# Performance work log

Measured on AMD Instinct MI355X. Metric: run time of the kernel, lower is better.

## Reference

```python
import jax, jax.numpy as jnp
import numpy as np

N_USERS = 100000
N_ITEMS = 50000
N_LAYERS = 3
LATENT_DIM = 64
N_INTERACTIONS = 600000
BATCH = 4096
N_TOTAL = N_USERS + N_ITEMS


def setup_inputs() -> dict:
    key = jax.random.key(0)
    k_e, k_u, k_p, k_n = jax.random.split(key, 4)

    # --- build bipartite interaction graph (numpy, host-side like scipy in the original) ---
    rng = np.random.default_rng(0)
    u = rng.integers(0, N_USERS, size=N_INTERACTIONS)
    i = rng.integers(0, N_ITEMS, size=N_INTERACTIONS) + N_USERS
    # symmetrize: A[u, i] = 1 and A[i, u] = 1
    row = np.concatenate([u, i]).astype(np.int32)
    col = np.concatenate([i, u]).astype(np.int32)
    # symmetric degree normalization: D^{-1/2} A D^{-1/2}
    deg = np.bincount(row, minlength=N_TOTAL).astype(np.float32)
    d_inv = np.power(deg + 1e-9, -0.5)
    d_inv[np.isinf(d_inv)] = 0.0
    vals = (d_inv[row] * d_inv[col]).astype(np.float32)

    # Xavier-uniform init for E0 (fan_in = fan_out = dims of the weight matrix)
    limit = float(np.sqrt(6.0 / (N_TOTAL + LATENT_DIM)))
    E0 = jax.random.uniform(k_e, (N_TOTAL, LATENT_DIM), jnp.float32, -limit, limit)

    return {
        "users": jax.random.randint(k_u, (BATCH,), 0, N_USERS),
        "pos_items": jax.random.randint(k_p, (BATCH,), 0, N_ITEMS),
        "neg_items": jax.random.randint(k_n, (BATCH,), 0, N_ITEMS),
        "E0": E0,
        "adj_row": jnp.asarray(row),
        "adj_col": jnp.asarray(col),
        "adj_vals": jnp.asarray(vals),
    }


def reference(users, pos_items, neg_items, E0, adj_row, adj_col, adj_vals):
    # SpMM via gather + segment-sum: out[r] = sum_{e: row[e]=r} vals[e] * E[col[e]]
    def spmm(E):
        return jax.ops.segment_sum(adj_vals[:, None] * E[adj_col], adj_row,
                                   num_segments=N_TOTAL)

    # layer propagation with running sum (mean over layer stack)
    E_k = E0
    acc = E0
    for _ in range(N_LAYERS):
        E_k = spmm(E_k)
        acc = acc + E_k
    final_emb = acc / (N_LAYERS + 1)  # [N_TOTAL, D]

    user_emb = final_emb[:N_USERS]
    item_emb = final_emb[N_USERS:]

    u_emb = user_emb[users]
    pos_emb = item_emb[pos_items]
    neg_emb = item_emb[neg_items]
    u_emb0 = E0[users]
    pos_emb0 = E0[N_USERS + pos_items]
    neg_emb0 = E0[N_USERS + neg_items]
    return (u_emb, pos_emb, neg_emb, u_emb0, pos_emb0, neg_emb0)
```

## Files before the change

### kernel.cpp

```cpp
#include <hip/hip_runtime.h>
#include <hip/hip_fp16.h>

#define LATENT 64
#define N_USERS_C 100000

#define BROWS 128
#define LOG_BROWS 7
#define NBUCK_MAX 1280
#define NBLKA_MAX 512
#define SORT_T 256
#define SORT_E 16
#define SORT_CHUNK (SORT_T * SORT_E)
#define BUCK_CAP 4608

__device__ __forceinline__ unsigned enc_val14(float v) {
    unsigned vb = (unsigned)__float_as_int(v) + 0x1000u;
    return (((vb >> 23) - 0x77u) << 10) | ((vb >> 13) & 0x3FFu);
}
__device__ __forceinline__ float dec_val14(unsigned m) {
    return __uint_as_float(m ? ((((m >> 10) + 0x77u) << 23) | ((m & 0x3FFu) << 13)) : 0u);
}


__global__ void sortA_kernel(const int* __restrict__ row, const int* __restrict__ col,
                             const float* __restrict__ vals,
                             unsigned* __restrict__ aux, unsigned char* __restrict__ rowloc,
                             int* __restrict__ cntmat, int* __restrict__ srcmat,
                             int* __restrict__ bcnt, int nnz, int nbuck) {
    __shared__ int cnt[NBUCK_MAX];
    __shared__ int off[NBUCK_MAX];
    __shared__ int part[SORT_T];
    __shared__ unsigned buf[SORT_CHUNK];
    __shared__ unsigned char rbuf[SORT_CHUNK];
    int t = threadIdx.x, blk = blockIdx.x;
    int base = blk * SORT_CHUNK;

    for (int i = t; i < nbuck; i += SORT_T) cnt[i] = 0;
    __syncthreads();

    int      eb[SORT_E];
    unsigned pl[SORT_E];
    unsigned char rl8[SORT_E];
#pragma unroll
    for (int j = 0; j < SORT_E; j++) {
        int e = base + j * SORT_T + t;
        if (e < nnz) {
            int r = row[e];
            int b = r >> LOG_BROWS;
            eb[j] = b;
            pl[j] = (unsigned)col[e] | (enc_val14(vals[e]) << 18);
            rl8[j] = (unsigned char)(r & (BROWS - 1));
            atomicAdd(&cnt[b], 1);
        } else {
            eb[j] = -1;
        }
    }
    __syncthreads();

    int chunk = (nbuck + SORT_T - 1) / SORT_T;
    int lo = t * chunk, hi = lo + chunk; if (hi > nbuck) hi = nbuck;
    int s = 0;
    for (int i = lo; i < hi; i++) s += cnt[i];
    part[t] = s;
    __syncthreads();
    for (int o = 1; o < SORT_T; o <<= 1) {
        int x = (t >= o) ? part[t - o] : 0;
        __syncthreads();
        part[t] += x;
        __syncthreads();
    }
    int run = (t == 0) ? 0 : part[t - 1];
    for (int i = lo; i < hi; i++) { off[i] = run; run += cnt[i]; }
    __syncthreads();

#pragma unroll
    for (int j = 0; j < SORT_E; j++) {
        if (eb[j] >= 0) {
            int p = atomicAdd(&off[eb[j]], 1);
            buf[p] = pl[j];
            rbuf[p] = rl8[j];
        }
    }
    __syncthreads();

    for (int b = t; b < nbuck; b += SORT_T) {
        int c = cnt[b];
        int beg = off[b] - c;
        cntmat[(size_t)blk * nbuck + b] = c;
        srcmat[(size_t)blk * nbuck + b] = beg;
        if (c) atomicAdd(&bcnt[b], c);
    }
    int nvalid = nnz - base; if (nvalid > SORT_CHUNK) nvalid = SORT_CHUNK;
    for (int i = t; i < nvalid; i += SORT_T) {
        aux[base + i] = buf[i];
        rowloc[base + i] = rbuf[i];
    }
}


__global__ void bscan_kernel(const int* __restrict__ bcnt, int* __restrict__ bstart,
                             int nbuck) {
    __shared__ int part[SORT_T];
    int t = threadIdx.x;
    int chunk = (nbuck + SORT_T - 1) / SORT_T;
    int lo = t * chunk, hi = lo + chunk; if (hi > nbuck) hi = nbuck;
    int s = 0;
    for (int i = lo; i < hi; i++) s += bcnt[i];
    part[t] = s;
    __syncthreads();
    for (int o = 1; o < SORT_T; o <<= 1) {
        int x = (t >= o) ? part[t - o] : 0;
        __syncthreads();
        part[t] += x;
        __syncthreads();
    }
    int run = (t == 0) ? 0 : part[t - 1];
    for (int i = lo; i < hi; i++) { bstart[i] = run; run += bcnt[i]; }
    if (t == SORT_T - 1) bstart[nbuck] = run;
}


__global__ void sortB_kernel(const unsigned* __restrict__ aux,
                             const unsigned char* __restrict__ rowloc,
                             const int* __restrict__ cntmat, const int* __restrict__ srcmat,
                             const int* __restrict__ bstart,
                             unsigned* __restrict__ edges, int* __restrict__ startOut,
                             int* __restrict__ origRow, int* __restrict__ slotOfRow,
                             int nblkA, int nbuck, int ntotal, int nnz) {
    __shared__ int rs[NBLKA_MAX], roff[NBLKA_MAX + 1];
    __shared__ int part[SORT_T];
    __shared__ unsigned buf[BUCK_CAP];
    __shared__ unsigned char rbuf[BUCK_CAP];
    __shared__ int cnt128[BROWS];
    __shared__ int slotOf[BROWS];
    __shared__ int rowOf[BROWS];
    __shared__ int offS[BROWS];
    __shared__ int placeOff[BROWS];
    __shared__ int dhist[64];
    int b = blockIdx.x, t = threadIdx.x;
    int base = bstart[b];
    int tot = bstart[b + 1] - base;
    int rbase = b * BROWS;
    int nr = ntotal - rbase; if (nr > BROWS) nr = BROWS;

    int chunk = (nblkA + SORT_T - 1) / SORT_T;
    int lo = t * chunk, hi = lo + chunk; if (hi > nblkA) hi = nblkA;
    int rcl[8];
    int s = 0;
    for (int i = lo; i < hi; i++) {
        int c = cntmat[(size_t)i * nbuck + b];
        rcl[i - lo] = c;
        rs[i] = srcmat[(size_t)i * nbuck + b];
        s += c;
    }
    part[t] = s;
    if (t < BROWS) cnt128[t] = 0;
    if (t < 64) dhist[t] = 0;
    __syncthreads();
    for (int o = 1; o < SORT_T; o <<= 1) {
        int x = (t >= o) ? part[t - o] : 0;
        __syncthreads();
        part[t] += x;
        __syncthreads();
    }
    int run = (t == 0) ? 0 : part[t - 1];
    for (int i = lo; i < hi; i++) { roff[i] = run; run += rcl[i - lo]; }
    if (t == SORT_T - 1) roff[nblkA] = part[SORT_T - 1];
    __syncthreads();

    for (int i = t; i < tot; i += SORT_T) {
        int lo2 = 0, hi2 = nblkA;
        while (hi2 - lo2 > 1) {
            int mid = (lo2 + hi2) >> 1;
            if (roff[mid] <= i) lo2 = mid; else hi2 = mid;
        }
        size_t src = (size_t)lo2 * SORT_CHUNK + rs[lo2] + (i - roff[lo2]);
        buf[i] = aux[src];
        unsigned char rl = rowloc[src];
        rbuf[i] = rl;
        atomicAdd(&cnt128[rl], 1);
    }
    __syncthreads();

    if (t < nr) { int d = min(cnt128[t], 63); atomicAdd(&dhist[d], 1); }
    __syncthreads();
    part[t] = (t < 64) ? dhist[t] : 0;
    __syncthreads();
    for (int o = 1; o < 64; o <<= 1) {
        int x = (t >= o) ? part[t - o] : 0;
        __syncthreads();
        part[t] += x;
        __syncthreads();
    }
    if (t < 64) dhist[t] = (t == 0) ? 0 : part[t - 1];
    __syncthreads();
    if (t < nr) {
        int d = min(cnt128[t], 63);
        int sl = atomicAdd(&dhist[d], 1);
        slotOf[t] = sl;
        rowOf[sl] = t;
    }
    __syncthreads();

    part[t] = (t < nr) ? cnt128[rowOf[t]] : 0;
    __syncthreads();
    for (int o = 1; o < SORT_T; o <<= 1) {
        int x = (t >= o) ? part[t - o] : 0;
        __syncthreads();
        part[t] += x;
        __syncthreads();
    }
    if (t < nr) offS[t] = (t == 0) ? 0 : part[t - 1];
    __syncthreads();

    if (t < nr) {
        startOut[rbase + t]   = base + offS[t];
        origRow[rbase + t]    = rbase + rowOf[t];
        slotOfRow[rbase + t]  = rbase + slotOf[t];
        placeOff[t] = offS[slotOf[t]];
    }
    if (b == nbuck - 1 && t == 0) startOut[ntotal] = nnz;
    __syncthreads();

    for (int i = t; i < tot; i += SORT_T) {
        int p = atomicAdd(&placeOff[rbuf[i]], 1);
        edges[base + p] = buf[i];
    }
}

__global__ void conv_kernel(const float* __restrict__ in, __half* __restrict__ outh, int n4) {
    int i = blockIdx.x * blockDim.x + threadIdx.x;
    if (i >= n4) return;
    float4 v = ((const float4*)in)[i];
    __half2* o = (__half2*)outh;
    o[2 * i]     = __floats2half2_rn(v.x, v.y);
    o[2 * i + 1] = __floats2half2_rn(v.z, v.w);
}


__global__ void spmm_slot(const int* __restrict__ start, const int* __restrict__ origRow,
                          const unsigned* __restrict__ edges,
                          const __half* __restrict__ Ein, __half* __restrict__ Eout,
                          int nslots) {
    int t = blockIdx.x * blockDim.x + threadIdx.x;
    int w = t >> 6;
    int lane = t & 63;
    int g = lane >> 4, l = lane & 15;
    int s = 4 * w + g;
    if (s >= nslots) return;
    int b = start[s];
    int e = start[s + 1];
    int ro = origRow[s];
    float a0 = 0.f, a1 = 0.f, a2 = 0.f, a3 = 0.f;
    for (int k = b; k < e; k += 4) {
        unsigned ed[4];
#pragma unroll
        for (int j = 0; j < 4; j++) {
            int kk = k + j;
            ed[j] = (kk < e) ? edges[kk] : 0u;
        }
        ushort4 gv[4];
#pragma unroll
        for (int j = 0; j < 4; j++) {
            gv[j] = *(const ushort4*)(Ein + (size_t)(ed[j] & 0x3FFFFu) * LATENT + 4 * l);
        }
#pragma unroll
        for (int j = 0; j < 4; j++) {
            float wv = dec_val14(ed[j] >> 18);
            const __half2* h2 = (const __half2*)&gv[j];
            a0 += wv * __low2float(h2[0]);
            a1 += wv * __high2float(h2[0]);
            a2 += wv * __low2float(h2[1]);
            a3 += wv * __high2float(h2[1]);
        }
    }
    union { ushort4 u; __half2 h[2]; } o;
    o.h[0] = __floats2half2_rn(a0, a1);
    o.h[1] = __floats2half2_rn(a2, a3);
    *(ushort4*)(Eout + (size_t)ro * LATENT + 4 * l) = o.u;
}


__global__ void fin_fused(const int* __restrict__ users, const int* __restrict__ pos,
                          const int* __restrict__ neg,
                          const int* __restrict__ start, const int* __restrict__ slotOfRow,
                          const unsigned* __restrict__ edges,
                          const float* __restrict__ E0, const __half* __restrict__ E1,
                          const __half* __restrict__ E2,
                          float* __restrict__ out, int batch) {
    int t = blockIdx.x * blockDim.x + threadIdx.x;
    int w = t >> 6;
    int lane = t & 63;
    int g = lane >> 4, l = lane & 15;
    int i = 4 * w + g;
    int nent = 3 * batch;
    if (i >= nent) return;
    int grp = i / batch;
    int bb = i - grp * batch;
    int r = (grp == 0) ? users[bb] : (grp == 1) ? (N_USERS_C + pos[bb]) : (N_USERS_C + neg[bb]);
    int s = slotOfRow[r];
    int b = start[s];
    int e = start[s + 1];
    float a0 = 0.f, a1 = 0.f, a2 = 0.f, a3 = 0.f;
    for (int k = b; k < e; k += 4) {
        unsigned ed[4];
#pragma unroll
        for (int j = 0; j < 4; j++) {
            int kk = k + j;
            ed[j] = (kk < e) ? edges[kk] : 0u;
        }
        ushort4 gv[4];
#pragma unroll
        for (int j = 0; j < 4; j++) {
            gv[j] = *(const ushort4*)(E2 + (size_t)(ed[j] & 0x3FFFFu) * LATENT + 4 * l);
        }
#pragma unroll
        for (int j = 0; j < 4; j++) {
            float wv = dec_val14(ed[j] >> 18);
            const __half2* h2 = (const __half2*)&gv[j];
            a0 += wv * __low2float(h2[0]);
            a1 += wv * __high2float(h2[0]);
            a2 += wv * __low2float(h2[1]);
            a3 += wv * __high2float(h2[1]);
        }
    }
    size_t idx = (size_t)r * LATENT + 4 * l;
    float4 e0v = *(const float4*)(E0 + idx);
    ushort4 e1u = *(const ushort4*)(E1 + idx);
    ushort4 e2u = *(const ushort4*)(E2 + idx);
    const __half2* h1 = (const __half2*)&e1u;
    const __half2* h2v = (const __half2*)&e2u;
    float4 res;
    res.x = 0.25f * (e0v.x + __low2float(h1[0])  + __low2float(h2v[0])  + a0);
    res.y = 0.25f * (e0v.y + __high2float(h1[0]) + __high2float(h2v[0]) + a1);
    res.z = 0.25f * (e0v.z + __low2float(h1[1])  + __low2float(h2v[1])  + a2);
    res.w = 0.25f * (e0v.w + __high2float(h1[1]) + __high2float(h2v[1]) + a3);
    int total = nent * LATENT;
    *(float4*)(out + (size_t)i * LATENT + 4 * l) = res;
    *(float4*)(out + total + (size_t)i * LATENT + 4 * l) = e0v;
}

extern "C" void kernel_launch(void* const* d_in, const int* in_sizes, int n_in,
                              void* d_out, int out_size, void* d_ws, size_t ws_size,
                              hipStream_t stream) {
    const int*   users = (const int*)d_in[0];
    const int*   pos   = (const int*)d_in[1];
    const int*   neg   = (const int*)d_in[2];
    const float* E0    = (const float*)d_in[3];
    const int*   row   = (const int*)d_in[4];
    const int*   col   = (const int*)d_in[5];
    const float* vals  = (const float*)d_in[6];
    float*       out   = (float*)d_out;

    const int batch  = in_sizes[0];
    const int nnz    = in_sizes[4];
    const int ntotal = in_sizes[3] / LATENT;
    const int nbuck  = (ntotal + BROWS - 1) / BROWS;
    const int nblkA  = (nnz + SORT_CHUNK - 1) / SORT_CHUNK;

    auto align256 = [](size_t x) { return (x + 255) & ~(size_t)255; };

    const size_t hbufBytes = align256((size_t)ntotal * LATENT * sizeof(__half));
    const size_t edgeBytes = align256((size_t)nnz * sizeof(unsigned));
    const size_t auxBytes  = align256((size_t)nnz * sizeof(unsigned));
    const size_t matBytes  = align256((size_t)nblkA * nbuck * sizeof(int));
    const size_t stBytes   = align256((size_t)(ntotal + 1) * sizeof(int));
    const size_t bsBytes   = align256((size_t)(nbuck + 1) * sizeof(int));

    char* p = (char*)d_ws;
    __half* E0h      = (__half*)p;          p += hbufBytes;
    __half* bufA     = (__half*)p;          p += hbufBytes;
    __half* bufB     = (__half*)p;          p += hbufBytes;
    __half* bufC     = (__half*)p;          p += hbufBytes;
    unsigned* edges  = (unsigned*)p;        p += edgeBytes;
    int*    startA   = (int*)p;             p += stBytes;
    int*    origRow  = (int*)p;             p += stBytes;
    int*    slotOfRw = (int*)p;             p += stBytes;
    int*    bstart   = (int*)p;             p += bsBytes;
    int*    bcnt     = (int*)p;             p += bsBytes;
    unsigned*      aux    = (unsigned*)bufC;
    unsigned char* rowloc = (unsigned char*)((char*)bufC + auxBytes);
    int* cntmat = (int*)bufB;
    int* srcmat = (int*)((char*)bufB + matBytes);

    hipMemsetAsync(bcnt, 0, (size_t)nbuck * sizeof(int), stream);

    const int threads = 256;
    const int slotWaves = (ntotal + 3) / 4;
    const int spBlocks = (slotWaves * 64 + threads - 1) / threads;
    const int nent = 3 * batch;
    const int fBlocks = (((nent + 3) / 4) * 64 + threads - 1) / threads;
    const int n4 = ntotal * LATENT / 4;
    const int cBlocks = (n4 + threads - 1) / threads;

    sortA_kernel<<<nblkA, SORT_T, 0, stream>>>(row, col, vals, aux, rowloc,
                                               cntmat, srcmat, bcnt, nnz, nbuck);
    bscan_kernel<<<1, SORT_T, 0, stream>>>(bcnt, bstart, nbuck);
    conv_kernel<<<cBlocks, threads, 0, stream>>>(E0, E0h, n4);
    sortB_kernel<<<nbuck, SORT_T, 0, stream>>>(aux, rowloc, cntmat, srcmat, bstart,
                                               edges, startA, origRow, slotOfRw,
                                               nblkA, nbuck, ntotal, nnz);

    spmm_slot<<<spBlocks, threads, 0, stream>>>(startA, origRow, edges, E0h, bufA, ntotal);
    spmm_slot<<<spBlocks, threads, 0, stream>>>(startA, origRow, edges, bufA, bufB, ntotal);
    fin_fused<<<fBlocks, threads, 0, stream>>>(users, pos, neg, startA, slotOfRw, edges,
                                               E0, bufA, bufB, out, batch);
}
```

Baseline: 206.6 us.

## Fuse fp16 conversion into sortA, fold bucket scan into sortB, widen SpMM gathers

Adds the E0 fp32-to-fp16 conversion as extra blocks inside the sortA launch and drops the single-block bucket scan kernel. Each sortB block now computes its own bucket base with a block-wide prefix over bcnt. This removes two launches and the serialization a one-block kernel imposes. The SpMM kernel now uses 8 lanes per row with 16-byte gathers instead of 16 lanes with 8-byte gathers, which halves the work items and doubles per-lane accumulators. The costs are redundant scan work in every sortB block and fewer lanes in flight per row.

Result: faster. 190.0 us (-8.0%).

```diff
diff --git a/kernel.cpp b/kernel.cpp
--- a/kernel.cpp
+++ b/kernel.cpp
@@ -13,6 +13,8 @@
 #define SORT_CHUNK (SORT_T * SORT_E)
 #define BUCK_CAP 4608
 
+typedef unsigned short ushort8_t __attribute__((ext_vector_type(8)));
+
 __device__ __forceinline__ unsigned enc_val14(float v) {
     unsigned vb = (unsigned)__float_as_int(v) + 0x1000u;
     return (((vb >> 23) - 0x77u) << 10) | ((vb >> 13) & 0x3FFu);
@@ -22,17 +24,37 @@
 }
 
 
-__global__ void sortA_kernel(const int* __restrict__ row, const int* __restrict__ col,
-                             const float* __restrict__ vals,
-                             unsigned* __restrict__ aux, unsigned char* __restrict__ rowloc,
-                             int* __restrict__ cntmat, int* __restrict__ srcmat,
-                             int* __restrict__ bcnt, int nnz, int nbuck) {
+__global__ void sortA_conv_kernel(const int* __restrict__ row, const int* __restrict__ col,
+                                  const float* __restrict__ vals,
+                                  unsigned* __restrict__ aux, unsigned char* __restrict__ rowloc,
+                                  int* __restrict__ cntmat, int* __restrict__ srcmat,
+                                  int* __restrict__ bcnt, int nnz, int nbuck, int nblkA,
+                                  const float* __restrict__ E0, __half* __restrict__ E0h,
+                                  int n4) {
     __shared__ int cnt[NBUCK_MAX];
     __shared__ int off[NBUCK_MAX];
     __shared__ int part[SORT_T];
     __shared__ unsigned buf[SORT_CHUNK];
     __shared__ unsigned char rbuf[SORT_CHUNK];
-    int t = threadIdx.x, blk = blockIdx.x;
+    int t = threadIdx.x;
+
+    if (blockIdx.x >= nblkA) {
+        int cb = blockIdx.x - nblkA;
+        int base4 = cb * (SORT_T * 4);
+#pragma unroll
+        for (int jj = 0; jj < 4; jj++) {
+            int i = base4 + jj * SORT_T + t;
+            if (i < n4) {
+                float4 v = ((const float4*)E0)[i];
+                __half2* o = (__half2*)E0h;
+                o[2 * i]     = __floats2half2_rn(v.x, v.y);
+                o[2 * i + 1] = __floats2half2_rn(v.z, v.w);
+            }
+        }
+        return;
+    }
+
+    int blk = blockIdx.x;
     int base = blk * SORT_CHUNK;
 
     for (int i = t; i < nbuck; i += SORT_T) cnt[i] = 0;
@@ -98,32 +120,10 @@
 }
 
 
-__global__ void bscan_kernel(const int* __restrict__ bcnt, int* __restrict__ bstart,
-                             int nbuck) {
-    __shared__ int part[SORT_T];
-    int t = threadIdx.x;
-    int chunk = (nbuck + SORT_T - 1) / SORT_T;
-    int lo = t * chunk, hi = lo + chunk; if (hi > nbuck) hi = nbuck;
-    int s = 0;
-    for (int i = lo; i < hi; i++) s += bcnt[i];
-    part[t] = s;
-    __syncthreads();
-    for (int o = 1; o < SORT_T; o <<= 1) {
-        int x = (t >= o) ? part[t - o] : 0;
-        __syncthreads();
-        part[t] += x;
-        __syncthreads();
-    }
-    int run = (t == 0) ? 0 : part[t - 1];
-    for (int i = lo; i < hi; i++) { bstart[i] = run; run += bcnt[i]; }
-    if (t == SORT_T - 1) bstart[nbuck] = run;
-}
-
-
 __global__ void sortB_kernel(const unsigned* __restrict__ aux,
                              const unsigned char* __restrict__ rowloc,
                              const int* __restrict__ cntmat, const int* __restrict__ srcmat,
-                             const int* __restrict__ bstart,
+                             const int* __restrict__ bcnt,
                              unsigned* __restrict__ edges, int* __restrict__ startOut,
                              int* __restrict__ origRow, int* __restrict__ slotOfRow,
                              int nblkA, int nbuck, int ntotal, int nnz) {
@@ -138,8 +138,21 @@
     __shared__ int placeOff[BROWS];
     __shared__ int dhist[64];
     int b = blockIdx.x, t = threadIdx.x;
-    int base = bstart[b];
-    int tot = bstart[b + 1] - base;
+
+    int sb = 0;
+    for (int i = t; i < b; i += SORT_T) sb += bcnt[i];
+    part[t] = sb;
+    __syncthreads();
+    for (int o = 1; o < SORT_T; o <<= 1) {
+        int x = (t >= o) ? part[t - o] : 0;
+        __syncthreads();
+        part[t] += x;
+        __syncthreads();
+    }
+    int base = part[SORT_T - 1];
+    int tot = bcnt[b];
+    __syncthreads();
+
     int rbase = b * BROWS;
     int nr = ntotal - rbase; if (nr > BROWS) nr = BROWS;
 
@@ -228,15 +241,6 @@
     }
 }
 
-__global__ void conv_kernel(const float* __restrict__ in, __half* __restrict__ outh, int n4) {
-    int i = blockIdx.x * blockDim.x + threadIdx.x;
-    if (i >= n4) return;
-    float4 v = ((const float4*)in)[i];
-    __half2* o = (__half2*)outh;
-    o[2 * i]     = __floats2half2_rn(v.x, v.y);
-    o[2 * i + 1] = __floats2half2_rn(v.z, v.w);
-}
-
 
 __global__ void spmm_slot(const int* __restrict__ start, const int* __restrict__ origRow,
                           const unsigned* __restrict__ edges,
@@ -245,13 +249,14 @@
     int t = blockIdx.x * blockDim.x + threadIdx.x;
     int w = t >> 6;
     int lane = t & 63;
-    int g = lane >> 4, l = lane & 15;
-    int s = 4 * w + g;
+    int g = lane >> 3, l = lane & 7;
+    int s = 8 * w + g;
     if (s >= nslots) return;
     int b = start[s];
     int e = start[s + 1];
     int ro = origRow[s];
     float a0 = 0.f, a1 = 0.f, a2 = 0.f, a3 = 0.f;
+    float a4 = 0.f, a5 = 0.f, a6 = 0.f, a7 = 0.f;
     for (int k = b; k < e; k += 4) {
         unsigned ed[4];
 #pragma unroll
@@ -259,10 +264,10 @@
             int kk = k + j;
             ed[j] = (kk < e) ? edges[kk] : 0u;
         }
-        ushort4 gv[4];
-#pragma unroll
-        for (int j = 0; j < 4; j++) {
-            gv[j] = *(const ushort4*)(Ein + (size_t)(ed[j] & 0x3FFFFu) * LATENT + 4 * l);
+        ushort8_t gv[4];
+#pragma unroll
+        for (int j = 0; j < 4; j++) {
+            gv[j] = *(const ushort8_t*)(Ein + (size_t)(ed[j] & 0x3FFFFu) * LATENT + 8 * l);
         }
 #pragma unroll
         for (int j = 0; j < 4; j++) {
@@ -272,12 +277,18 @@
             a1 += wv * __high2float(h2[0]);
             a2 += wv * __low2float(h2[1]);
             a3 += wv * __high2float(h2[1]);
-        }
-    }
-    union { ushort4 u; __half2 h[2]; } o;
+            a4 += wv * __low2float(h2[2]);
+            a5 += wv * __high2float(h2[2]);
+            a6 += wv * __low2float(h2[3]);
+            a7 += wv * __high2float(h2[3]);
+        }
+    }
+    union { ushort8_t u; __half2 h[4]; } o;
     o.h[0] = __floats2half2_rn(a0, a1);
     o.h[1] = __floats2half2_rn(a2, a3);
-    *(ushort4*)(Eout + (size_t)ro * LATENT + 4 * l) = o.u;
+    o.h[2] = __floats2half2_rn(a4, a5);
+    o.h[3] = __floats2half2_rn(a6, a7);
+    *(ushort8_t*)(Eout + (size_t)ro * LATENT + 8 * l) = o.u;
 }
 
 
@@ -376,7 +387,6 @@
     int*    startA   = (int*)p;             p += stBytes;
     int*    origRow  = (int*)p;             p += stBytes;
     int*    slotOfRw = (int*)p;             p += stBytes;
-    int*    bstart   = (int*)p;             p += bsBytes;
     int*    bcnt     = (int*)p;             p += bsBytes;
     unsigned*      aux    = (unsigned*)bufC;
     unsigned char* rowloc = (unsigned char*)((char*)bufC + auxBytes);
@@ -386,18 +396,17 @@
     hipMemsetAsync(bcnt, 0, (size_t)nbuck * sizeof(int), stream);
 
     const int threads = 256;
-    const int slotWaves = (ntotal + 3) / 4;
+    const int slotWaves = (ntotal + 7) / 8;
     const int spBlocks = (slotWaves * 64 + threads - 1) / threads;
     const int nent = 3 * batch;
     const int fBlocks = (((nent + 3) / 4) * 64 + threads - 1) / threads;
     const int n4 = ntotal * LATENT / 4;
-    const int cBlocks = (n4 + threads - 1) / threads;
-
-    sortA_kernel<<<nblkA, SORT_T, 0, stream>>>(row, col, vals, aux, rowloc,
-                                               cntmat, srcmat, bcnt, nnz, nbuck);
-    bscan_kernel<<<1, SORT_T, 0, stream>>>(bcnt, bstart, nbuck);
-    conv_kernel<<<cBlocks, threads, 0, stream>>>(E0, E0h, n4);
-    sortB_kernel<<<nbuck, SORT_T, 0, stream>>>(aux, rowloc, cntmat, srcmat, bstart,
+    const int cBlocks4 = (n4 + SORT_T * 4 - 1) / (SORT_T * 4);
+
+    sortA_conv_kernel<<<nblkA + cBlocks4, SORT_T, 0, stream>>>(
+        row, col, vals, aux, rowloc, cntmat, srcmat, bcnt, nnz, nbuck, nblkA,
+        E0, E0h, n4);
+    sortB_kernel<<<nbuck, SORT_T, 0, stream>>>(aux, rowloc, cntmat, srcmat, bcnt,
                                                edges, startA, origRow, slotOfRw,
                                                nblkA, nbuck, ntotal, nnz);
 
```
